# Kernel optimization log

Hardware: AMD Instinct MI355X
Metric: run time of the kernel (lower is better)

The kernel has to match this reference:

```python
import jax, jax.numpy as jnp
import numpy as np

D1, D2 = 64, 64          # degree1, degree2
BW1, BW2 = 3, 3          # bandwidths
WIDTH = 64


def dst_mat(n):
    # Orthonormal DST-I matrix: self-inverse, stand-in for sp.WSWA / sp.sin_transform.
    k = np.arange(1, n + 1)
    M = np.sqrt(2.0 / (n + 1)) * np.sin(np.pi * np.outer(k, k) / (n + 1))
    return jnp.asarray(M, jnp.float32)


def transform2d(x, S_row, S_col):
    # apply spectral transform along last axis then axis -2 (T_pipe with axes [-1,-2])
    x = jnp.einsum('bcij,jk->bcik', x, S_col)
    return jnp.einsum('ki,bcij->bckj', S_row, x)


def wswano(u, w, out_ch):
    # WSWANO.forward: transform -> quasi-diag (unfold+einsum) multiply -> zero-pad -> inverse transform
    B, C, Nx, Ny = u.shape
    S1, S2 = dst_mat(Ny), dst_mat(Nx)
    a = transform2d(u, S2, S1)
    ap = a[:, :, :D1 + BW1 - 1, :D2 + BW2 - 1]
    # torch.nn.Unfold(kernel=(bw1,bw2)): patches ordered (c, ki, kj) x row-major positions
    patches = jnp.stack([ap[:, :, i:i + D1, j:j + D2]
                         for i in range(BW1) for j in range(BW2)], axis=2)  # [B,C,bw1*bw2,D1,D2]
    xp = patches.reshape(B, C * BW1 * BW2, D1 * D2)
    out = jnp.einsum('bix,iox->box', xp, w)  # quasi-diagonal spectral multiply
    b = jnp.zeros((B, out_ch, Nx, Ny), u.dtype).at[:, :, :D1, :D2].set(
        out.reshape(B, out_ch, D1, D2))
    return transform2d(b, S2, S1)  # DST-I is self-inverse => iT_pipe


def conv1x1(x, w, b):
    return jnp.einsum('bchw,oc->bohw', x, w) + b[None, :, None, None]


def gelu(x):
    return jax.nn.gelu(x, approximate=False)


def setup_inputs():
    key = jax.random.key(0)
    ks = jax.random.split(key, 18)
    B, Nx, Ny, W = 16, 128, 128, WIDTH

    def cw(k, cin, cout):
        return (2.0 / (cin + cout)) * jax.random.uniform(
            k, (cin * BW1 * BW2, cout, D1 * D2), jnp.float32)

    return {
        'x': jax.random.normal(ks[0], (B, Nx, Ny, 3), jnp.float32),
        'convl_w': cw(ks[1], 3, W - 3),
        'conv0_w': cw(ks[2], W, W),
        'conv1_w': cw(ks[3], W, W),
        'conv2_w': cw(ks[4], W, W),
        'conv3_w': cw(ks[5], W, W),
        'w0_w': 0.02 * jax.random.normal(ks[6], (W, W), jnp.float32),
        'w0_b': 0.02 * jax.random.normal(ks[7], (W,), jnp.float32),
        'w1_w': 0.02 * jax.random.normal(ks[8], (W, W), jnp.float32),
        'w1_b': 0.02 * jax.random.normal(ks[9], (W,), jnp.float32),
        'w2_w': 0.02 * jax.random.normal(ks[10], (W, W), jnp.float32),
        'w2_b': 0.02 * jax.random.normal(ks[11], (W,), jnp.float32),
        'w3_w': 0.02 * jax.random.normal(ks[12], (W, W), jnp.float32),
        'w3_b': 0.02 * jax.random.normal(ks[13], (W,), jnp.float32),
        'fc1_w': 0.02 * jax.random.normal(ks[14], (W, 128), jnp.float32),
        'fc1_b': 0.02 * jax.random.normal(ks[15], (128,), jnp.float32),
        'fc2_w': 0.02 * jax.random.normal(ks[16], (128, 1), jnp.float32),
        'fc2_b': 0.02 * jax.random.normal(ks[17], (1,), jnp.float32),
    }


def reference(x, convl_w, conv0_w, conv1_w, conv2_w, conv3_w,
              w0_w, w0_b, w1_w, w1_b, w2_w, w2_b, w3_w, w3_b,
              fc1_w, fc1_b, fc2_w, fc2_b):
    x = jnp.transpose(x, (0, 3, 1, 2))                       # [B,3,Nx,Ny]
    x = jnp.concatenate([x, gelu(wswano(x, convl_w, WIDTH - 3))], axis=1)
    for ww, wb, cw_ in ((w0_w, w0_b, conv0_w), (w1_w, w1_b, conv1_w),
                        (w2_w, w2_b, conv2_w), (w3_w, w3_b, conv3_w)):
        x = x + gelu(conv1x1(x, ww, wb) + wswano(x, cw_, WIDTH))  # skip + GELU block
    x = jnp.transpose(x, (0, 2, 3, 1))                       # [B,Nx,Ny,width]
    x = gelu(x @ fc1_w + fc1_b)
    return x @ fc2_w + fc2_b                                  # [B,Nx,Ny,1]
```

## Files before the change

kernel.cpp:

```cpp
#include <hip/hip_runtime.h>
#include <math.h>

#define NB 16
#define NN 128
#define WC 64
#define DD 64
#define NP 66

typedef float v4f __attribute__((ext_vector_type(4)));
typedef unsigned int u32;

__device__ __forceinline__ float gelu_f(float x) {
    return 0.5f * x * (1.0f + erff(x * 0.70710678118654752f));
}

__device__ __forceinline__ void gload16(const float* g, float* l) {
    __builtin_amdgcn_global_load_lds(
        (const __attribute__((address_space(1))) u32*)g,
        (__attribute__((address_space(3))) u32*)l, 16, 0, 0);
}

__global__ void k_dst(float* __restrict__ S) {
    int idx = blockIdx.x * 256 + threadIdx.x;
    int k = idx >> 7, j = idx & 127;
    double arg = 3.14159265358979323846 * (double)((k + 1) * (j + 1)) / 129.0;
    S[idx] = (float)(sqrt(2.0 / 129.0) * sin(arg));
}

__global__ void k_tin(const float* __restrict__ in, float* __restrict__ xc) {
    int idx = blockIdx.x * 256 + threadIdx.x;
    int j = idx & 127;
    int i = (idx >> 7) & 127;
    int t = idx >> 14;
    int b = t / 3, c = t - b * 3;
    xc[(((size_t)b * WC + c) << 14) + i * 128 + j] =
        in[((size_t)(b * 128 + i) * 128 + j) * 3 + c];
}

__global__ __launch_bounds__(256) void k_tfwd66(const float* __restrict__ Xg,
                                                float* __restrict__ Yc,
                                                const float* __restrict__ Sg,
                                                int Cact) {
    __shared__ float sSt[80 * 132];
    __shared__ float sU[66 * 132];
    int bid = blockIdx.x;
    int b = bid / Cact, c = bid - b * Cact;
    const float* X = Xg + (((size_t)b * WC + c) << 14);
    int tid = threadIdx.x;
    int tx = tid & 15, ty = tid >> 4;
    for (int l = tid; l < 80 * 128; l += 256)
        sSt[(l >> 7) * 132 + (l & 127)] = Sg[l];
    float acc[8][5];
#pragma unroll
    for (int r = 0; r < 8; ++r)
#pragma unroll
        for (int q = 0; q < 5; ++q) acc[r][q] = 0.f;
    for (int jh = 0; jh < 2; ++jh) {
        __syncthreads();
        for (int l = tid; l < 8192; l += 256)
            sU[(l >> 6) * 68 + (l & 63)] = X[((l >> 6) << 7) + jh * 64 + (l & 63)];
        __syncthreads();
        for (int jj = 0; jj < 64; jj += 4) {
            float4 xv[8], sv[5];
#pragma unroll
            for (int r = 0; r < 8; ++r)
                xv[r] = *(const float4*)&sU[(ty + 16 * r) * 68 + jj];
#pragma unroll
            for (int q = 0; q < 5; ++q)
                sv[q] = *(const float4*)&sSt[(tx + 16 * q) * 132 + jh * 64 + jj];
#pragma unroll
            for (int r = 0; r < 8; ++r)
#pragma unroll
                for (int q = 0; q < 5; ++q) {
                    acc[r][q] += xv[r].x * sv[q].x;
                    acc[r][q] += xv[r].y * sv[q].y;
                    acc[r][q] += xv[r].z * sv[q].z;
                    acc[r][q] += xv[r].w * sv[q].w;
                }
        }
    }
    __syncthreads();
#pragma unroll
    for (int q = 0; q < 5; ++q) {
        int k = tx + 16 * q;
        if (k < 66) {
#pragma unroll
            for (int r = 0; r < 8; ++r)
                sU[k * 132 + ty + 16 * r] = acc[r][q];
        }
    }
    __syncthreads();
    float a2[5][5];
#pragma unroll
    for (int r = 0; r < 5; ++r)
#pragma unroll
        for (int q = 0; q < 5; ++q) a2[r][q] = 0.f;
    for (int i0 = 0; i0 < 128; i0 += 4) {
        float4 sv[5], tv[5];
#pragma unroll
        for (int r = 0; r < 5; ++r)
            sv[r] = *(const float4*)&sSt[(ty + 16 * r) * 132 + i0];
#pragma unroll
        for (int q = 0; q < 5; ++q) {
            int m = tx + 16 * q;
            if (m < 66) tv[q] = *(const float4*)&sU[m * 132 + i0];
            else { tv[q].x = 0.f; tv[q].y = 0.f; tv[q].z = 0.f; tv[q].w = 0.f; }
        }
#pragma unroll
        for (int r = 0; r < 5; ++r)
#pragma unroll
            for (int q = 0; q < 5; ++q) {
                a2[r][q] += sv[r].x * tv[q].x;
                a2[r][q] += sv[r].y * tv[q].y;
                a2[r][q] += sv[r].z * tv[q].z;
                a2[r][q] += sv[r].w * tv[q].w;
            }
    }
    float* Y = Yc + (size_t)(b * WC + c) * 4488;
#pragma unroll
    for (int r = 0; r < 5; ++r) {
        int kk = ty + 16 * r;
        if (kk < 66) {
#pragma unroll
            for (int q = 0; q < 5; ++q) {
                int m = tx + 16 * q;
                if (m < 66) Y[kk * 68 + m] = a2[r][q];
            }
        }
    }
}

__global__ __launch_bounds__(256) void k_tinv(const float* __restrict__ Op,
                                              float* __restrict__ Yg,
                                              const float* __restrict__ Sg,
                                              int Cact, int ncc, int ch_off, int do_gelu) {
    __shared__ float sS[64 * 128];
    __shared__ float sXT[64 * 132];
    int bid = blockIdx.x;
    int b = bid / Cact, c = bid - b * Cact;
    const float* X = Op + ((size_t)(b * WC + c) << 12);
    const size_t cstride = (size_t)NB * WC * 4096;
    float* Y = Yg + (((size_t)b * WC + c + ch_off) << 14);
    int tid = threadIdx.x;
    for (int l = tid; l < 8192; l += 256) sS[l] = Sg[l];
    for (int l = tid; l < 4096; l += 256) {
        int r = l >> 6, q = l & 63;
        float v = X[l];
        for (int cc = 1; cc < ncc; ++cc) v += X[cc * cstride + l];
        sXT[r * 65 + q] = v;
    }
    __syncthreads();
    int cg = tid & 7;
    int rg = tid >> 3;
    v4f a1[2][4];
#pragma unroll
    for (int r = 0; r < 2; ++r)
#pragma unroll
        for (int m = 0; m < 4; ++m) {
            a1[r][m].x = 0.f; a1[r][m].y = 0.f; a1[r][m].z = 0.f; a1[r][m].w = 0.f;
        }
    for (int j = 0; j < 64; ++j) {
        float x0 = sXT[(rg * 2 + 0) * 65 + j];
        float x1 = sXT[(rg * 2 + 1) * 65 + j];
#pragma unroll
        for (int m = 0; m < 4; ++m) {
            v4f sv = *(const v4f*)&sS[j * 128 + cg * 4 + 32 * m];
            a1[0][m] += sv * x0;
            a1[1][m] += sv * x1;
        }
    }
    __syncthreads();
#pragma unroll
    for (int r = 0; r < 2; ++r)
#pragma unroll
        for (int m = 0; m < 4; ++m)
            *(v4f*)&sXT[(rg * 2 + r) * 132 + cg * 4 + 32 * m] = a1[r][m];
    __syncthreads();
    v4f a2[4][4];
#pragma unroll
    for (int r = 0; r < 4; ++r)
#pragma unroll
        for (int m = 0; m < 4; ++m) {
            a2[r][m].x = 0.f; a2[r][m].y = 0.f; a2[r][m].z = 0.f; a2[r][m].w = 0.f;
        }
    for (int i = 0; i < 64; ++i) {
        v4f sv = *(const v4f*)&sS[i * 128 + rg * 4];
        v4f tv[4];
#pragma unroll
        for (int m = 0; m < 4; ++m)
            tv[m] = *(const v4f*)&sXT[i * 132 + cg * 4 + 32 * m];
#pragma unroll
        for (int m = 0; m < 4; ++m) {
            a2[0][m] += tv[m] * sv.x;
            a2[1][m] += tv[m] * sv.y;
            a2[2][m] += tv[m] * sv.z;
            a2[3][m] += tv[m] * sv.w;
        }
    }
#pragma unroll
    for (int r = 0; r < 4; ++r) {
        int row = rg * 4 + r;
#pragma unroll
        for (int m = 0; m < 4; ++m) {
            v4f v = a2[r][m];
            if (do_gelu) {
                v.x = gelu_f(v.x); v.y = gelu_f(v.y);
                v.z = gelu_f(v.z); v.w = gelu_f(v.w);
            }
            *(v4f*)&Y[row * 128 + cg * 4 + 32 * m] = v;
        }
    }
}

__global__ __launch_bounds__(256, 2) void k_mix6(const float* __restrict__ Ac,
                                                 const float* __restrict__ Wt,
                                                 float* __restrict__ Op,
                                                 int Cin, int Cout, int cper) {
    __shared__ __align__(16) float sa[2][16 * 4 * 68];
    int bx = blockIdx.x;
    int ocb = blockIdx.y;
    int ccb = blockIdx.z;
    int c0 = ccb * cper;
    int c1 = c0 + cper; if (c1 > Cin) c1 = Cin;
    int tid = threadIdx.x;
    int ocl = tid & 7, yq = (tid >> 3) & 15, xh = tid >> 7;
    int x = bx * 2 + xh;
    int oc = ocb * 8 + ocl;
    bool ocok = oc < Cout;
    v4f z4; z4.x = 0.f; z4.y = 0.f; z4.z = 0.f; z4.w = 0.f;

    const size_t wstep = (size_t)Cout * 4096;
    const float* wbase = Wt + (size_t)(ocok ? oc : 0) * 4096 + x * 64 + (yq << 2);

    int gbase[5];
#pragma unroll
    for (int k = 0; k < 5; ++k) {
        int f = 4 * tid + 1024 * k;
        int fv = (f < 4352) ? f : 0;
        int bb = fv / 272; int off = fv - bb * 272;
        gbase[k] = bb * (WC * 4488) + bx * 136 + off;
    }

    float acc[16][4];
#pragma unroll
    for (int bb = 0; bb < 16; ++bb)
#pragma unroll
        for (int k = 0; k < 4; ++k) acc[bb][k] = 0.f;

    {
        const float* src = Ac + (size_t)c0 * 4488;
#pragma unroll
        for (int k = 0; k < 4; ++k)
            gload16(src + gbase[k], &sa[0][4 * tid + 1024 * k]);
        if (tid < 64) gload16(src + gbase[4], &sa[0][4 * tid + 4096]);
    }
    v4f wvA[9];
#pragma unroll
    for (int t = 0; t < 9; ++t)
        wvA[t] = ocok ? __builtin_nontemporal_load(
                            (const v4f*)(wbase + ((size_t)c0 * 9 + t) * wstep))
                      : z4;
    __syncthreads();

    int cur = 0;
    for (int c = c0; c < c1; ++c) {
        bool hn = (c + 1) < c1;
        v4f wvN[9];
        if (hn) {
            float* dst = sa[cur ^ 1];
            const float* src = Ac + (size_t)(c + 1) * 4488;
#pragma unroll
            for (int k = 0; k < 4; ++k)
                gload16(src + gbase[k], dst + 4 * tid + 1024 * k);
            if (tid < 64) gload16(src + gbase[4], dst + 4 * tid + 4096);
#pragma unroll
            for (int t = 0; t < 9; ++t)
                wvN[t] = ocok ? __builtin_nontemporal_load(
                                    (const v4f*)(wbase + ((size_t)(c + 1) * 9 + t) * wstep))
                              : z4;
        }
        const float* sab = sa[cur];
#pragma unroll
        for (int pi = 0; pi < 3; ++pi) {
#pragma unroll
            for (int bb = 0; bb < 16; ++bb) {
                const float* sp = &sab[(bb * 4 + xh + pi) * 68 + (yq << 2)];
                float4 s0 = *(const float4*)sp;
                float2 s1 = *(const float2*)(sp + 4);
                float sv[6] = {s0.x, s0.y, s0.z, s0.w, s1.x, s1.y};
#pragma unroll
                for (int k = 0; k < 4; ++k)
#pragma unroll
                    for (int pj = 0; pj < 3; ++pj)
                        acc[bb][k] = fmaf(sv[k + pj], wvA[pi * 3 + pj][k], acc[bb][k]);
            }
        }
        if (hn) {
            __syncthreads();
#pragma unroll
            for (int t = 0; t < 9; ++t) wvA[t] = wvN[t];
            cur ^= 1;
        }
    }

    if (ocok) {
        float* Opc = Op + (size_t)ccb * ((size_t)NB * WC * 4096);
#pragma unroll
        for (int bb = 0; bb < 16; ++bb) {
            float4 o4;
            o4.x = acc[bb][0]; o4.y = acc[bb][1];
            o4.z = acc[bb][2]; o4.w = acc[bb][3];
            *(float4*)&Opc[(((size_t)bb * WC + oc) << 12) + x * 64 + (yq << 2)] = o4;
        }
    }
}

__global__ __launch_bounds__(256) void k_blockup(float* __restrict__ xc,
                                                 const float* __restrict__ sp,
                                                 const float* __restrict__ wmat,
                                                 const float* __restrict__ bias) {
    __shared__ float sw[64 * 64];
    __shared__ float sx[128 * 65];
    __shared__ float sb[64];
    int bi = blockIdx.x;
    int b = bi >> 7, i = bi & 127;
    int tid = threadIdx.x;
    for (int l = tid; l < 4096; l += 256) sw[l] = wmat[l];
    if (tid < 64) sb[tid] = bias[tid];
    for (int l = tid; l < 8192; l += 256) {
        int c = l >> 7, j = l & 127;
        sx[j * 65 + c] = xc[(((size_t)b * WC + c) << 14) + i * 128 + j];
    }
    __syncthreads();
    int j = tid & 127, h = tid >> 7;
    float xr[64];
#pragma unroll
    for (int c = 0; c < 64; ++c) xr[c] = sx[j * 65 + c];
#pragma unroll 2
    for (int o = 0; o < 32; ++o) {
        int oc = h * 32 + o;
        float a = sb[oc];
#pragma unroll
        for (int c4 = 0; c4 < 16; ++c4) {
            v4f w4 = *(const v4f*)&sw[oc * 64 + c4 * 4];
            a = fmaf(xr[c4 * 4 + 0], w4.x, a);
            a = fmaf(xr[c4 * 4 + 1], w4.y, a);
            a = fmaf(xr[c4 * 4 + 2], w4.z, a);
            a = fmaf(xr[c4 * 4 + 3], w4.w, a);
        }
        size_t gi = (((size_t)b * WC + oc) << 14) + i * 128 + j;
        float v = a + sp[gi];
        xc[gi] = sx[j * 65 + oc] + gelu_f(v);
    }
}

__global__ __launch_bounds__(256) void k_fc(const float* __restrict__ xc,
                                            const float* __restrict__ W1,
                                            const float* __restrict__ b1,
                                            const float* __restrict__ W2,
                                            const float* __restrict__ b2,
                                            float* __restrict__ out) {
    __shared__ float sW1T[128 * 68];
    __shared__ float sx[128 * 65];
    __shared__ float sW2[128];
    __shared__ float sb1[128];
    __shared__ float spart[256];
    int bi = blockIdx.x; int b = bi >> 7, i = bi & 127;
    int tid = threadIdx.x;
    for (int l = tid; l < 8192; l += 256) {
        int c = l >> 7, oo = l & 127;
        sW1T[oo * 68 + c] = W1[l];
    }
    if (tid < 128) { sW2[tid] = W2[tid]; sb1[tid] = b1[tid]; }
    for (int l = tid; l < 8192; l += 256) {
        int c = l >> 7, j = l & 127;
        sx[j * 65 + c] = xc[(((size_t)b * WC + c) << 14) + i * 128 + j];
    }
    __syncthreads();
    int j = tid & 127, h = tid >> 7;
    float xr[64];
#pragma unroll
    for (int c = 0; c < 64; ++c) xr[c] = sx[j * 65 + c];
    float part = 0.f;
#pragma unroll 2
    for (int o = 0; o < 64; ++o) {
        int oo = h * 64 + o;
        float a = sb1[oo];
#pragma unroll
        for (int c4 = 0; c4 < 16; ++c4) {
            v4f w4 = *(const v4f*)&sW1T[oo * 68 + c4 * 4];
            a = fmaf(xr[c4 * 4 + 0], w4.x, a);
            a = fmaf(xr[c4 * 4 + 1], w4.y, a);
            a = fmaf(xr[c4 * 4 + 2], w4.z, a);
            a = fmaf(xr[c4 * 4 + 3], w4.w, a);
        }
        part += gelu_f(a) * sW2[oo];
    }
    spart[j * 2 + h] = part;
    __syncthreads();
    if (h == 0) out[(size_t)bi * 128 + j] = spart[j * 2] + spart[j * 2 + 1] + b2[0];
}

extern "C" void kernel_launch(void* const* d_in, const int* in_sizes, int n_in,
                              void* d_out, int out_size, void* d_ws, size_t ws_size,
                              hipStream_t stream) {
    (void)in_sizes; (void)n_in; (void)out_size; (void)ws_size;
    const float* x_in    = (const float*)d_in[0];
    const float* convl_w = (const float*)d_in[1];
    const float* conv_w[4] = {(const float*)d_in[2], (const float*)d_in[3],
                              (const float*)d_in[4], (const float*)d_in[5]};
    const float* ww[4] = {(const float*)d_in[6], (const float*)d_in[8],
                          (const float*)d_in[10], (const float*)d_in[12]};
    const float* wb[4] = {(const float*)d_in[7], (const float*)d_in[9],
                          (const float*)d_in[11], (const float*)d_in[13]};
    const float* fc1w = (const float*)d_in[14];
    const float* fc1b = (const float*)d_in[15];
    const float* fc2w = (const float*)d_in[16];
    const float* fc2b = (const float*)d_in[17];
    float* out = (float*)d_out;

    float* S   = (float*)d_ws;
    float* xc  = S + 16384;
    float* t1  = xc + (size_t)NB * WC * 16384;
    float* tA  = t1 + (size_t)NB * WC * 16384;
    float* Op  = tA + (size_t)NB * WC * 4488;

    k_dst<<<64, 256, 0, stream>>>(S);
    k_tin<<<3072, 256, 0, stream>>>(x_in, xc);

    k_tfwd66<<<NB * 3, 256, 0, stream>>>(xc, tA, S, 3);
    k_mix6<<<dim3(32, 8, 1), 256, 0, stream>>>(tA, convl_w, Op, 3, 61, 3);
    k_tinv<<<NB * 61, 256, 0, stream>>>(Op, xc, S, 61, 1, 3, 1);

    for (int L = 0; L < 4; ++L) {
        k_tfwd66<<<NB * WC, 256, 0, stream>>>(xc, tA, S, WC);
        k_mix6<<<dim3(32, 8, 2), 256, 0, stream>>>(tA, conv_w[L], Op, WC, WC, 32);
        k_tinv<<<NB * WC, 256, 0, stream>>>(Op, t1, S, WC, 2, 0, 0);
        k_blockup<<<2048, 256, 0, stream>>>(xc, t1, ww[L], wb[L]);
    }

    k_fc<<<2048, 256, 0, stream>>>(xc, fc1w, fc1b, fc2w, fc2b, out);
}
```

Before: 1.676 ms.

## Exploit DST-I even/odd symmetry in inverse transform to halve FLOPs

```diff
diff --git a/kernel.cpp b/kernel.cpp
--- a/kernel.cpp
+++ b/kernel.cpp
@@ -130,11 +130,11 @@
     }
 }
 
-__global__ __launch_bounds__(256) void k_tinv(const float* __restrict__ Op,
-                                              float* __restrict__ Yg,
-                                              const float* __restrict__ Sg,
-                                              int Cact, int ncc, int ch_off, int do_gelu) {
-    __shared__ float sS[64 * 128];
+__global__ __launch_bounds__(256, 3) void k_tinv(const float* __restrict__ Op,
+                                                 float* __restrict__ Yg,
+                                                 const float* __restrict__ Sg,
+                                                 int Cact, int ncc, int ch_off, int do_gelu) {
+    __shared__ float sS[64 * 64];
     __shared__ float sXT[64 * 132];
     int bid = blockIdx.x;
     int b = bid / Cact, c = bid - b * Cact;
@@ -142,72 +142,83 @@
     const size_t cstride = (size_t)NB * WC * 4096;
     float* Y = Yg + (((size_t)b * WC + c + ch_off) << 14);
     int tid = threadIdx.x;
-    for (int l = tid; l < 8192; l += 256) sS[l] = Sg[l];
+    for (int l = tid; l < 4096; l += 256)
+        sS[l] = Sg[((l >> 6) << 7) + (l & 63)];
     for (int l = tid; l < 4096; l += 256) {
         int r = l >> 6, q = l & 63;
         float v = X[l];
         for (int cc = 1; cc < ncc; ++cc) v += X[cc * cstride + l];
-        sXT[r * 65 + q] = v;
+        sXT[r * 66 + q] = v;
     }
     __syncthreads();
     int cg = tid & 7;
     int rg = tid >> 3;
-    v4f a1[2][4];
+    v4f aP[2][2], aM[2][2];
 #pragma unroll
     for (int r = 0; r < 2; ++r)
 #pragma unroll
+        for (int m = 0; m < 2; ++m) {
+            aP[r][m].x = 0.f; aP[r][m].y = 0.f; aP[r][m].z = 0.f; aP[r][m].w = 0.f;
+            aM[r][m].x = 0.f; aM[r][m].y = 0.f; aM[r][m].z = 0.f; aM[r][m].w = 0.f;
+        }
+    for (int jp = 0; jp < 32; ++jp) {
+        float2 x0 = *(const float2*)&sXT[(rg * 2 + 0) * 66 + 2 * jp];
+        float2 x1 = *(const float2*)&sXT[(rg * 2 + 1) * 66 + 2 * jp];
+#pragma unroll
+        for (int m = 0; m < 2; ++m) {
+            v4f se = *(const v4f*)&sS[(2 * jp) * 64 + cg * 4 + 32 * m];
+            v4f so = *(const v4f*)&sS[(2 * jp + 1) * 64 + cg * 4 + 32 * m];
+            aP[0][m] += se * x0.x;  aM[0][m] += so * x0.y;
+            aP[1][m] += se * x1.x;  aM[1][m] += so * x1.y;
+        }
+    }
+    __syncthreads();
+#pragma unroll
+    for (int r = 0; r < 2; ++r)
+#pragma unroll
+        for (int m = 0; m < 2; ++m) {
+            v4f tlo = aP[r][m] + aM[r][m];
+            v4f td  = aP[r][m] - aM[r][m];
+            v4f thi; thi.x = td.w; thi.y = td.z; thi.z = td.y; thi.w = td.x;
+            int row = rg * 2 + r;
+            *(v4f*)&sXT[row * 132 + cg * 4 + 32 * m] = tlo;
+            *(v4f*)&sXT[row * 132 + 124 - cg * 4 - 32 * m] = thi;
+        }
+    __syncthreads();
+    v4f p2[2][4], m2[2][4];
+#pragma unroll
+    for (int r = 0; r < 2; ++r)
+#pragma unroll
         for (int m = 0; m < 4; ++m) {
-            a1[r][m].x = 0.f; a1[r][m].y = 0.f; a1[r][m].z = 0.f; a1[r][m].w = 0.f;
-        }
-    for (int j = 0; j < 64; ++j) {
-        float x0 = sXT[(rg * 2 + 0) * 65 + j];
-        float x1 = sXT[(rg * 2 + 1) * 65 + j];
+            p2[r][m].x = 0.f; p2[r][m].y = 0.f; p2[r][m].z = 0.f; p2[r][m].w = 0.f;
+            m2[r][m].x = 0.f; m2[r][m].y = 0.f; m2[r][m].z = 0.f; m2[r][m].w = 0.f;
+        }
+    for (int ip = 0; ip < 32; ++ip) {
+        float2 sve = *(const float2*)&sS[(2 * ip) * 64 + rg * 2];
+        float2 svo = *(const float2*)&sS[(2 * ip + 1) * 64 + rg * 2];
 #pragma unroll
         for (int m = 0; m < 4; ++m) {
-            v4f sv = *(const v4f*)&sS[j * 128 + cg * 4 + 32 * m];
-            a1[0][m] += sv * x0;
-            a1[1][m] += sv * x1;
-        }
-    }
-    __syncthreads();
-#pragma unroll
-    for (int r = 0; r < 2; ++r)
-#pragma unroll
-        for (int m = 0; m < 4; ++m)
-            *(v4f*)&sXT[(rg * 2 + r) * 132 + cg * 4 + 32 * m] = a1[r][m];
-    __syncthreads();
-    v4f a2[4][4];
-#pragma unroll
-    for (int r = 0; r < 4; ++r)
+            v4f te = *(const v4f*)&sXT[(2 * ip) * 132 + cg * 4 + 32 * m];
+            v4f to = *(const v4f*)&sXT[(2 * ip + 1) * 132 + cg * 4 + 32 * m];
+            p2[0][m] += te * sve.x;  p2[1][m] += te * sve.y;
+            m2[0][m] += to * svo.x;  m2[1][m] += to * svo.y;
+        }
+    }
+#pragma unroll
+    for (int r = 0; r < 2; ++r) {
+        int rlo = rg * 2 + r, rhi = 127 - rlo;
 #pragma unroll
         for (int m = 0; m < 4; ++m) {
-            a2[r][m].x = 0.f; a2[r][m].y = 0.f; a2[r][m].z = 0.f; a2[r][m].w = 0.f;
-        }
-    for (int i = 0; i < 64; ++i) {
-        v4f sv = *(const v4f*)&sS[i * 128 + rg * 4];
-        v4f tv[4];
-#pragma unroll
-        for (int m = 0; m < 4; ++m)
-            tv[m] = *(const v4f*)&sXT[i * 132 + cg * 4 + 32 * m];
-#pragma unroll
-        for (int m = 0; m < 4; ++m) {
-            a2[0][m] += tv[m] * sv.x;
-            a2[1][m] += tv[m] * sv.y;
-            a2[2][m] += tv[m] * sv.z;
-            a2[3][m] += tv[m] * sv.w;
-        }
-    }
-#pragma unroll
-    for (int r = 0; r < 4; ++r) {
-        int row = rg * 4 + r;
-#pragma unroll
-        for (int m = 0; m < 4; ++m) {
-            v4f v = a2[r][m];
+            v4f ylo = p2[r][m] + m2[r][m];
+            v4f yhi = p2[r][m] - m2[r][m];
             if (do_gelu) {
-                v.x = gelu_f(v.x); v.y = gelu_f(v.y);
-                v.z = gelu_f(v.z); v.w = gelu_f(v.w);
+                ylo.x = gelu_f(ylo.x); ylo.y = gelu_f(ylo.y);
+                ylo.z = gelu_f(ylo.z); ylo.w = gelu_f(ylo.w);
+                yhi.x = gelu_f(yhi.x); yhi.y = gelu_f(yhi.y);
+                yhi.z = gelu_f(yhi.z); yhi.w = gelu_f(yhi.w);
             }
-            *(v4f*)&Y[row * 128 + cg * 4 + 32 * m] = v;
+            *(v4f*)&Y[rlo * 128 + cg * 4 + 32 * m] = ylo;
+            *(v4f*)&Y[rhi * 128 + cg * 4 + 32 * m] = yhi;
         }
     }
 }
```

Result: faster. 1.606 ms, median of 3 (-4.2%).
